# Optimization experiments

Hardware: AMD Instinct MI355X
Metric: run time of the kernel (lower is better)

Reference implementation:

```python
import jax, jax.numpy as jnp
import numpy as np

SIGMAS = (0.02, 0.01, 0.008)   # self.sig
SIGMA_N = 0.5                  # self.sig_n
COORD_SCALE = 0.05             # keep distances commensurate with sigmas


def setup_inputs() -> dict:
    key = jax.random.key(0)
    k1, k2, k3 = jax.random.split(key, 3)
    B, Vn, Fn = 2, 5000, 6144
    predictions = jax.random.uniform(k1, (B, Vn, 3), dtype=jnp.float32) * COORD_SCALE
    targets = jax.random.uniform(k2, (B, Vn, 3), dtype=jnp.float32) * COORD_SCALE
    faces = jax.random.randint(k3, (Fn, 3), 0, Vn, dtype=jnp.int32)
    return {"predictions": predictions, "targets": targets, "faces": faces}


def _mesh_quantities(V, F):
    # face centers C [F,3], areas L [F,1], unit normals Nn [F,3]
    v0, v1, v2 = V[F[:, 0]], V[F[:, 1]], V[F[:, 2]]
    C = (v0 + v1 + v2) / 3.0
    N = 0.5 * jnp.cross(v1 - v0, v2 - v0)
    L = jnp.sqrt((N * N).sum(-1, keepdims=True) + 1e-24)
    return C, L, N / L


def _varifold_prod(C1, L1, N1, C2, L2, N2, sigma, sigma_n):
    # <mu1, mu2> = sum_ij L1_i L2_j exp(-|c_i-c_j|^2/sigma^2) exp((<n_i,n_j>-1)/sigma_n^2)
    d2 = ((C1[:, None, :] - C2[None, :, :]) ** 2).sum(-1)          # [F,F]
    ndot = N1 @ N2.T                                               # [F,F]
    K = jnp.exp(-d2 / (sigma * sigma) + (ndot - 1.0) / (sigma_n * sigma_n))
    return (L1[:, 0] * (K @ L2[:, 0])).sum()


def reference(predictions, targets, faces):
    def per_sample(Vs, Vt):
        Cs, Ls, Ns = _mesh_quantities(Vs, faces)
        Ct, Lt, Nt = _mesh_quantities(Vt, faces)
        li = jnp.float32(0.0)
        for sig in SIGMAS:  # small fixed set of sigmas
            w = (sig / SIGMAS[0]) ** 2
            pss = _varifold_prod(Cs, Ls, Ns, Cs, Ls, Ns, sig, SIGMA_N)
            pst = _varifold_prod(Cs, Ls, Ns, Ct, Lt, Nt, sig, SIGMA_N)
            ptt = _varifold_prod(Ct, Lt, Nt, Ct, Lt, Nt, sig, SIGMA_N)
            li = li + w * (pss - 2.0 * pst + ptt)
        return li

    L = jax.vmap(per_sample)(predictions, targets)  # [B]
    return jnp.mean(L)
```

## Files before the change

### kernel.cpp

```cpp
#include <hip/hip_runtime.h>

#define F_FACES 6144
#define VN      5000
#define BATCH   2

#define SC_F    30.02806022f
#define SN_F    2.40224481f
#define C4_F    5.7707801635558535f

__device__ __forceinline__ float fast_exp2(float x) {
    float r;
    asm("v_exp_f32 %0, %1" : "=v"(r) : "v"(x));
    return r;
}

__global__ __launch_bounds__(256) void mesh_prep(
    const float* __restrict__ pred, const float* __restrict__ targ,
    const int* __restrict__ faces, float4* __restrict__ ws4,
    float* __restrict__ out)
{
    const int f = blockIdx.x * 256 + threadIdx.x;
    const int m = blockIdx.y;
    if (blockIdx.x == 0 && m == 0 && threadIdx.x == 0) out[0] = 0.0f;
    if (f >= F_FACES) return;

    const int b = m >> 1, which = m & 1;
    const float* V = (which ? targ : pred) + b * (VN * 3);

    const int i0 = faces[3 * f + 0];
    const int i1 = faces[3 * f + 1];
    const int i2 = faces[3 * f + 2];

    const float v0x = V[3 * i0 + 0], v0y = V[3 * i0 + 1], v0z = V[3 * i0 + 2];
    const float v1x = V[3 * i1 + 0], v1y = V[3 * i1 + 1], v1z = V[3 * i1 + 2];
    const float v2x = V[3 * i2 + 0], v2y = V[3 * i2 + 1], v2z = V[3 * i2 + 2];

    const float Cx = (v0x + v1x + v2x) * (1.0f / 3.0f);
    const float Cy = (v0y + v1y + v2y) * (1.0f / 3.0f);
    const float Cz = (v0z + v1z + v2z) * (1.0f / 3.0f);

    const float e1x = v1x - v0x, e1y = v1y - v0y, e1z = v1z - v0z;
    const float e2x = v2x - v0x, e2y = v2y - v0y, e2z = v2z - v0z;

    const float Nx = 0.5f * (e1y * e2z - e1z * e2y);
    const float Ny = 0.5f * (e1z * e2x - e1x * e2z);
    const float Nz = 0.5f * (e1x * e2y - e1y * e2x);

    const float l2  = Nx * Nx + Ny * Ny + Nz * Nz + 1e-24f;
    const float L   = sqrtf(l2);
    const float inv = 1.0f / L;

    const float Csx = Cx * SC_F, Csy = Cy * SC_F, Csz = Cz * SC_F;
    const float a   = -(Csx * Csx + Csy * Csy + Csz * Csz);
    const float s   = inv * SN_F;

    const long base = (long)(m * F_FACES + f) * 2;
    ws4[base + 0] = make_float4(Csx, Csy, Csz, a);
    ws4[base + 1] = make_float4(Nx * s, Ny * s, Nz * s, log2f(L) - C4_F);
}

#define IT        4
#define TJ        64
#define J_CHUNKS  (F_FACES / TJ)
#define I_TILES   (F_FACES / (256 * IT))
#define I_ROWS    (256 * IT)

__global__ __launch_bounds__(256) void varifold_pairs(
    const float4* __restrict__ ws4, float* __restrict__ out)
{
    __shared__ float4 sAB[2 * TJ];
    __shared__ float  red[4];

    const int tid = threadIdx.x;
    const int it  = blockIdx.x / J_CHUNKS;
    const int jc  = blockIdx.x % J_CHUNKS;
    const int cb  = blockIdx.y;
    const int b   = cb / 3, c = cb % 3;
    const int m1  = b * 2 + (c == 2 ? 1 : 0);
    const int m2  = b * 2 + (c >= 1 ? 1 : 0);

    const int iBase = it * I_ROWS;
    const int jBase = jc * TJ;

    float wOut;
    bool straddle = false;
    if (c == 1) {
        wOut = -1.0f;
    } else {
        if (jBase + TJ <= iBase) return;
        if (jBase >= iBase + I_ROWS) {
            wOut = 1.0f;
        } else {
            wOut = 0.5f;
            straddle = true;
        }
    }

    const float4* P1 = ws4 + (long)m1 * (F_FACES * 2);
    const float4* P2 = ws4 + (long)m2 * (F_FACES * 2);

    float C2x[IT], C2y[IT], C2z[IT], Ai[IT];
    float Nix[IT], Niy[IT], Niz[IT], Li[IT];
    float acc[IT];
    int   iIdx[IT];

#pragma unroll
    for (int k = 0; k < IT; ++k) {
        const int i = iBase + k * 256 + tid;
        iIdx[k] = i;
        const float4 A  = P1[2 * i + 0];
        const float4 Bv = P1[2 * i + 1];
        C2x[k] = 2.0f * A.x; C2y[k] = 2.0f * A.y; C2z[k] = 2.0f * A.z;
        Ai[k]  = A.w;
        Nix[k] = Bv.x; Niy[k] = Bv.y; Niz[k] = Bv.z;
        Li[k]  = fast_exp2(Bv.w + C4_F);
        acc[k] = 0.0f;
    }

    if (tid < 2 * TJ) sAB[tid] = P2[2 * jBase + tid];
    __syncthreads();

    if (!straddle) {
#pragma unroll 4
        for (int jj = 0; jj < TJ; ++jj) {
            const float4 a4 = sAB[2 * jj + 0];
            const float4 b4 = sAB[2 * jj + 1];
#pragma unroll
            for (int k = 0; k < IT; ++k) {
                float r = fmaf(C2x[k], a4.x, a4.w);
                r = fmaf(C2y[k], a4.y, r);
                r = fmaf(C2z[k], a4.z, r);
                const float t0 = fast_exp2(r + Ai[k]);
                float n = fmaf(Nix[k], b4.x, b4.w);
                n = fmaf(Niy[k], b4.y, n);
                n = fmaf(Niz[k], b4.z, n);
                const float en = fast_exp2(n);
                const float t2  = t0 * t0;
                const float t4  = t2 * t2;
                const float t8  = t4 * t4;
                const float t16 = t8 * t8;
                const float t24 = t16 * t8;
                const float t25 = t24 * t0;
                float p = fmaf(0.25f, t16, t4);
                p = fmaf(0.16f, t25, p);
                acc[k] = fmaf(en, p, acc[k]);
            }
        }
    } else {
#pragma unroll 4
        for (int jj = 0; jj < TJ; ++jj) {
            const float4 a4 = sAB[2 * jj + 0];
            const float4 b4 = sAB[2 * jj + 1];
            const int j = jBase + jj;
#pragma unroll
            for (int k = 0; k < IT; ++k) {
                float r = fmaf(C2x[k], a4.x, a4.w);
                r = fmaf(C2y[k], a4.y, r);
                r = fmaf(C2z[k], a4.z, r);
                const float t0 = fast_exp2(r + Ai[k]);
                float n = fmaf(Nix[k], b4.x, b4.w);
                n = fmaf(Niy[k], b4.y, n);
                n = fmaf(Niz[k], b4.z, n);
                const float en = fast_exp2(n);
                const float t2  = t0 * t0;
                const float t4  = t2 * t2;
                const float t8  = t4 * t4;
                const float t16 = t8 * t8;
                const float t24 = t16 * t8;
                const float t25 = t24 * t0;
                float p = fmaf(0.25f, t16, t4);
                p = fmaf(0.16f, t25, p);
                float f = (j > iIdx[k]) ? 2.0f : 0.0f;
                f = (j == iIdx[k]) ? 1.0f : f;
                acc[k] = fmaf(f * en, p, acc[k]);
            }
        }
    }

    float part = 0.0f;
#pragma unroll
    for (int k = 0; k < IT; ++k) part = fmaf(acc[k], Li[k], part);

#pragma unroll
    for (int off = 32; off; off >>= 1) part += __shfl_xor(part, off);
    if ((tid & 63) == 0) red[tid >> 6] = part;
    __syncthreads();
    if (tid == 0) atomicAdd(out, wOut * (red[0] + red[1] + red[2] + red[3]));
}

extern "C" void kernel_launch(void* const* d_in, const int* in_sizes, int n_in,
                              void* d_out, int out_size, void* d_ws, size_t ws_size,
                              hipStream_t stream) {
    const float* pred  = (const float*)d_in[0];
    const float* targ  = (const float*)d_in[1];
    const int*   faces = (const int*)d_in[2];
    float*       out   = (float*)d_out;
    float4*      ws4   = (float4*)d_ws;

    dim3 g1(F_FACES / 256, 2 * BATCH);
    mesh_prep<<<g1, 256, 0, stream>>>(pred, targ, faces, ws4, out);

    dim3 g2(I_TILES * J_CHUNKS, 3 * BATCH);
    varifold_pairs<<<g2, 256, 0, stream>>>(ws4, out);
}
```

Measured before the change: 140.0 us.

## Halve block size and launch only non-empty triangular tiles via compact grid

The pair kernel now uses 128-thread blocks with a 512-row i-tile. It launches a flat 1D grid that enumerates only the useful blocks: full rectangles for the cross term and upper-triangular tiles for the two self terms. Before, the self terms launched blocks that exited immediately. This removes those empty blocks and gives finer work granularity for load balance, at the cost of a small loop to decode tile indices and more blocks doing atomics.

```diff
diff --git a/kernel.cpp b/kernel.cpp
--- a/kernel.cpp
+++ b/kernel.cpp
@@ -61,40 +61,48 @@
 
 #define IT        4
 #define TJ        64
+#define BLK       128
 #define J_CHUNKS  (F_FACES / TJ)
-#define I_TILES   (F_FACES / (256 * IT))
-#define I_ROWS    (256 * IT)
-
-__global__ __launch_bounds__(256) void varifold_pairs(
+#define I_ROWS    (BLK * IT)
+#define I_TILES   (F_FACES / I_ROWS)
+#define N_ST      (I_TILES * J_CHUNKS)
+#define N_TRI     624
+#define N_BLOCKS  (2 * N_ST + 4 * N_TRI)
+
+__global__ __launch_bounds__(BLK) void varifold_pairs(
     const float4* __restrict__ ws4, float* __restrict__ out)
 {
     __shared__ float4 sAB[2 * TJ];
-    __shared__ float  red[4];
+    __shared__ float  red[2];
 
     const int tid = threadIdx.x;
-    const int it  = blockIdx.x / J_CHUNKS;
-    const int jc  = blockIdx.x % J_CHUNKS;
-    const int cb  = blockIdx.y;
-    const int b   = cb / 3, c = cb % 3;
-    const int m1  = b * 2 + (c == 2 ? 1 : 0);
-    const int m2  = b * 2 + (c >= 1 ? 1 : 0);
-
+
+    int c, b, it, jc;
+    {
+        const int bi = blockIdx.x;
+        if (bi < 2 * N_ST) {
+            c = 1; b = bi / N_ST;
+            const int lin = bi % N_ST;
+            it = lin / J_CHUNKS; jc = lin % J_CHUNKS;
+        } else {
+            const int r = bi - 2 * N_ST;
+            const int q = r / N_TRI;
+            c = (q & 2) ? 2 : 0; b = q & 1;
+            int lin = r - q * N_TRI;
+            it = 0;
+            int w = J_CHUNKS;
+            while (lin >= w) { lin -= w; ++it; w -= 8; }
+            jc = 8 * it + lin;
+        }
+    }
+
+    const int m1 = b * 2 + (c == 2 ? 1 : 0);
+    const int m2 = b * 2 + (c >= 1 ? 1 : 0);
     const int iBase = it * I_ROWS;
     const int jBase = jc * TJ;
 
-    float wOut;
-    bool straddle = false;
-    if (c == 1) {
-        wOut = -1.0f;
-    } else {
-        if (jBase + TJ <= iBase) return;
-        if (jBase >= iBase + I_ROWS) {
-            wOut = 1.0f;
-        } else {
-            wOut = 0.5f;
-            straddle = true;
-        }
-    }
+    const bool straddle = (c != 1) && (jc < 8 * (it + 1));
+    const float wOut = (c == 1) ? -1.0f : (straddle ? 0.5f : 1.0f);
 
     const float4* P1 = ws4 + (long)m1 * (F_FACES * 2);
     const float4* P2 = ws4 + (long)m2 * (F_FACES * 2);
@@ -106,7 +114,7 @@
 
 #pragma unroll
     for (int k = 0; k < IT; ++k) {
-        const int i = iBase + k * 256 + tid;
+        const int i = iBase + k * BLK + tid;
         iIdx[k] = i;
         const float4 A  = P1[2 * i + 0];
         const float4 Bv = P1[2 * i + 1];
@@ -117,7 +125,7 @@
         acc[k] = 0.0f;
     }
 
-    if (tid < 2 * TJ) sAB[tid] = P2[2 * jBase + tid];
+    sAB[tid] = P2[2 * jBase + tid];
     __syncthreads();
 
     if (!straddle) {
@@ -185,7 +193,7 @@
     for (int off = 32; off; off >>= 1) part += __shfl_xor(part, off);
     if ((tid & 63) == 0) red[tid >> 6] = part;
     __syncthreads();
-    if (tid == 0) atomicAdd(out, wOut * (red[0] + red[1] + red[2] + red[3]));
+    if (tid == 0) atomicAdd(out, wOut * (red[0] + red[1]));
 }
 
 extern "C" void kernel_launch(void* const* d_in, const int* in_sizes, int n_in,
@@ -200,6 +208,5 @@
     dim3 g1(F_FACES / 256, 2 * BATCH);
     mesh_prep<<<g1, 256, 0, stream>>>(pred, targ, faces, ws4, out);
 
-    dim3 g2(I_TILES * J_CHUNKS, 3 * BATCH);
-    varifold_pairs<<<g2, 256, 0, stream>>>(ws4, out);
-}
+    varifold_pairs<<<dim3(N_BLOCKS), dim3(BLK), 0, stream>>>(ws4, out);
+}
```

After: 136.1 us. -2.8%, faster.
